# Optimization experiments

Hardware: AMD Instinct MI355X
Metric: run time of the kernel (lower is better)

## Reference

```python
import jax, jax.numpy as jnp
import numpy as np

N_NODES = 100000
N_FEAT = 256
HIDDEN = 16
N_CLASSES = 16
N_EDGES = 3200000


def setup_inputs() -> dict:
    key = jax.random.key(0)
    k = jax.random.split(key, 7)
    x = jax.random.normal(k[0], (N_NODES, N_FEAT), dtype=jnp.float32)
    edge_index = jax.random.randint(k[1], (2, N_EDGES), 0, N_NODES, dtype=jnp.int32)
    # GCNConv: linear (no bias) + bias added after aggregation
    s1 = 1.0 / np.sqrt(N_FEAT)
    W1 = jax.random.uniform(k[2], (N_FEAT, HIDDEN), jnp.float32, -s1, s1)
    b1 = jnp.zeros((HIDDEN,), jnp.float32)
    # SAGEConv: lin_l (on aggregated neighbors, with bias) + lin_r (root)
    s2 = 1.0 / np.sqrt(HIDDEN)
    Wl = jax.random.uniform(k[3], (HIDDEN, N_CLASSES), jnp.float32, -s2, s2)
    Wr = jax.random.uniform(k[4], (HIDDEN, N_CLASSES), jnp.float32, -s2, s2)
    b2 = jax.random.uniform(k[5], (N_CLASSES,), jnp.float32, -s2, s2)
    return {"x": x, "edge_index": edge_index, "W1": W1, "b1": b1,
            "Wl": Wl, "Wr": Wr, "b2": b2}


def reference(x, edge_index, W1, b1, Wl, Wr, b2):
    N = x.shape[0]
    src, dst = edge_index[0], edge_index[1]

    # ---- GCNConv(num_features -> hidden): transform, add self-loops,
    # symmetric normalization, sum-aggregate, add bias ----
    h = x @ W1  # [N, H]
    loop = jnp.arange(N, dtype=src.dtype)
    src2 = jnp.concatenate([src, loop])
    dst2 = jnp.concatenate([dst, loop])
    ones = jnp.ones(src2.shape[0], dtype=h.dtype)
    deg = jax.ops.segment_sum(ones, dst2, num_segments=N)  # in-degree incl. self-loop
    dinv = jnp.where(deg > 0, jax.lax.rsqrt(deg), 0.0)
    norm = dinv[src2] * dinv[dst2]  # [E+N]
    msgs = h[src2] * norm[:, None]
    h1 = jax.ops.segment_sum(msgs, dst2, num_segments=N) + b1  # [N, H]

    # ---- SAGEConv(hidden -> num_classes, aggr='mean') ----
    cnt = jax.ops.segment_sum(jnp.ones(src.shape[0], dtype=h1.dtype), dst, num_segments=N)
    agg = jax.ops.segment_sum(h1[src], dst, num_segments=N)
    agg = agg / jnp.maximum(cnt, 1.0)[:, None]  # mean over neighbors
    out = agg @ Wl + h1 @ Wr + b2  # [N, C]

    return jax.nn.log_softmax(out, axis=1)
```

## Files before the change

### kernel.cpp

```cpp
#include <hip/hip_runtime.h>
#include <cstddef>

#define NF 256
#define NH 16
#define NC 16

#define BN    128
#define BSH   7
#define BMSK  127
#define CAP   4608
#define AVLEN 16
#define ACH   (256*AVLEN)
#define NBMAX 800

typedef __attribute__((ext_vector_type(8))) short bf16x8;
typedef __attribute__((ext_vector_type(4))) float f32x4;

__device__ inline short f2bf(float f) {
    union { float f; unsigned int u; } v; v.f = f;
    const unsigned int r = v.u + 0x7FFFu + ((v.u >> 16) & 1u);
    return (short)(r >> 16);
}
__device__ inline float bf2f(unsigned short u) {
    union { unsigned int i; float f; } v; v.i = ((unsigned int)u) << 16;
    return v.f;
}

__global__ __launch_bounds__(256) void fusedAG_kernel(
    const int* __restrict__ src, const int* __restrict__ dst,
    unsigned int* __restrict__ bfill, unsigned int* __restrict__ bpairs,
    const float* __restrict__ x, const float* __restrict__ W1,
    float* __restrict__ hs_u, int E, int NBK, int NCH, int GEMMB, int N)
{
    __shared__ unsigned int hist[NBMAX];
    __shared__ unsigned int sbase[NBMAX];
    __shared__ unsigned int reorder[ACH];
    __shared__ unsigned short wbid[ACH];
    __shared__ unsigned int wsum[4];

    const int tid = threadIdx.x;

    const int nInter = 2 * (NCH < GEMMB ? NCH : GEMMB);
    int msId = -1, gbId = -1;
    const int bi = (int)blockIdx.x;
    if (bi < nInter) {
        if (bi & 1) gbId = bi >> 1; else msId = bi >> 1;
    } else {
        const int r = bi - nInter;
        if (NCH > GEMMB) msId = (nInter >> 1) + r; else gbId = (nInter >> 1) + r;
    }

    if (msId >= 0) {
        for (int i = tid; i < NBMAX; i += 256) hist[i] = 0u;
        __syncthreads();

        const int base = msId * ACH;
        unsigned int pv[AVLEN];
        unsigned int ps[AVLEN];
        #pragma unroll
        for (int l = 0; l < AVLEN; ++l) {
            const int e = base + l * 256 + tid;
            if (e < E) {
                const unsigned int s = (unsigned int)src[e];
                const unsigned int d = (unsigned int)dst[e];
                const unsigned int b = d >> BSH;
                pv[l] = (s << BSH) | (d & BMSK);
                const unsigned int slot = atomicAdd(&hist[b], 1u);
                ps[l] = (slot << 10) | b;
            } else {
                ps[l] = 0xFFFFFFFFu;
            }
        }
        __syncthreads();

        {
            const int lane = tid & 63;
            const int wid  = tid >> 6;
            const int b0 = tid * 4;
            unsigned int h0 = (b0 + 0 < NBMAX) ? hist[b0 + 0] : 0u;
            unsigned int h1 = (b0 + 1 < NBMAX) ? hist[b0 + 1] : 0u;
            unsigned int h2 = (b0 + 2 < NBMAX) ? hist[b0 + 2] : 0u;
            unsigned int h3 = (b0 + 3 < NBMAX) ? hist[b0 + 3] : 0u;
            const unsigned int l0 = h0, l1 = l0 + h1, l2 = l1 + h2;
            const unsigned int s = l2 + h3;
            unsigned int ws = s;
            #pragma unroll
            for (int d = 1; d < 64; d <<= 1) {
                const unsigned int v = __shfl_up(ws, d, 64);
                if (lane >= d) ws += v;
            }
            if (lane == 63) wsum[wid] = ws;
            __syncthreads();
            unsigned int woff = 0;
            #pragma unroll
            for (int w = 0; w < 4; ++w) woff += (w < wid) ? wsum[w] : 0u;
            const unsigned int ebase = woff + (ws - s);
            if (b0 + 0 < NBMAX) sbase[b0 + 0] = ebase;
            if (b0 + 1 < NBMAX) sbase[b0 + 1] = ebase + l0;
            if (b0 + 2 < NBMAX) sbase[b0 + 2] = ebase + l1;
            if (b0 + 3 < NBMAX) sbase[b0 + 3] = ebase + l2;
        }
        const int cc = (base + ACH <= E) ? ACH : (E - base);
        __syncthreads();

        #pragma unroll
        for (int l = 0; l < AVLEN; ++l) {
            if (ps[l] != 0xFFFFFFFFu) {
                const unsigned int b = ps[l] & 1023u;
                const unsigned int i = sbase[b] + (ps[l] >> 10);
                reorder[i] = pv[l];
                wbid[i] = (unsigned short)b;
            }
        }
        __syncthreads();

        for (int i = tid; i < NBK; i += 256) {
            const unsigned int h = hist[i];
            const unsigned int g = h ? atomicAdd(&bfill[i], h) : 0u;
            hist[i] = g - sbase[i];
        }
        __syncthreads();

        for (int i = tid; i < cc; i += 256) {
            const unsigned int b = wbid[i];
            const unsigned int g = hist[b] + (unsigned int)i;
            if (g < CAP) bpairs[(size_t)b * CAP + g] = reorder[i];
        }
    } else {
        const int lane = tid & 63;
        const int wave = tid >> 6;
        const int quad = lane >> 4;
        const int mn   = lane & 15;

        bf16x8 bfrag[8];
        #pragma unroll
        for (int kc = 0; kc < 8; ++kc) {
            #pragma unroll
            for (int j = 0; j < 8; ++j) {
                const int k = kc * 32 + quad * 8 + j;
                bfrag[kc][j] = f2bf(W1[k * NH + mn]);
            }
        }

        #pragma unroll
        for (int t = 0; t < 2; ++t) {
            const int tile = gbId * 8 + wave * 2 + t;
            const int n0 = tile * 16;
            if (n0 >= N) break;

            f32x4 acc = {0.f, 0.f, 0.f, 0.f};
            const float* xrow = x + (size_t)(n0 + mn) * NF + quad * 8;
            #pragma unroll
            for (int kc = 0; kc < 8; ++kc) {
                const float4 lo = *(const float4*)(xrow + kc * 32);
                const float4 hi = *(const float4*)(xrow + kc * 32 + 4);
                bf16x8 af;
                af[0] = f2bf(lo.x); af[1] = f2bf(lo.y); af[2] = f2bf(lo.z); af[3] = f2bf(lo.w);
                af[4] = f2bf(hi.x); af[5] = f2bf(hi.y); af[6] = f2bf(hi.z); af[7] = f2bf(hi.w);
                acc = __builtin_amdgcn_mfma_f32_16x16x32_bf16(af, bfrag[kc], acc, 0, 0, 0);
            }

            #pragma unroll
            for (int r = 0; r < 4; ++r) {
                const int row = quad * 4 + r;
                hs_u[(size_t)(n0 + row) * NH + mn] = acc[r];
            }
        }
    }
}

__global__ __launch_bounds__(256) void bucketB_kernel(
    const unsigned int* __restrict__ bfill, unsigned int* __restrict__ bpairs,
    const float* __restrict__ hs_u,
    int* __restrict__ rowptr, int* __restrict__ cnt, float* __restrict__ dinv,
    unsigned short* __restrict__ hs_bf, int N)
{
    __shared__ unsigned int pairs[CAP];
    __shared__ unsigned int ssorted[CAP];
    __shared__ unsigned int hist[BN];
    __shared__ unsigned int scan[BN];
    __shared__ unsigned int cursor[BN];
    __shared__ float sdinv[BN];

    const int tid = threadIdx.x;
    const int b = blockIdx.x;
    const size_t bbase = (size_t)b * CAP;
    const int nodeBase = b * BN;
    unsigned int m = bfill[b]; if (m > CAP) m = CAP;

    if (tid < BN) hist[tid] = 0u;
    __syncthreads();

    for (unsigned int i = tid; i < m; i += 256) {
        const unsigned int p = bpairs[bbase + i];
        pairs[i] = p;
        atomicAdd(&hist[p & BMSK], 1u);
    }
    __syncthreads();

    if (tid < BN) scan[tid] = hist[tid];
    __syncthreads();
    for (int off = 1; off < BN; off <<= 1) {
        unsigned int v = 0;
        if (tid < BN && tid >= off) v = scan[tid - off];
        __syncthreads();
        if (tid < BN) scan[tid] += v;
        __syncthreads();
    }
    if (tid < BN) cursor[tid] = scan[tid] - hist[tid];
    __syncthreads();

    for (unsigned int i = tid; i < m; i += 256) {
        const unsigned int p = pairs[i];
        const unsigned int pos = atomicAdd(&cursor[p & BMSK], 1u);
        ssorted[pos] = p >> BSH;
    }
    __syncthreads();

    for (unsigned int i = tid; i < m; i += 256)
        bpairs[bbase + i] = ssorted[i];

    if (tid < BN) {
        const int n = nodeBase + tid;
        const unsigned int h = hist[tid];
        const float dv = rsqrtf((float)h + 1.0f);
        sdinv[tid] = dv;
        if (n < N) {
            cnt[n] = (int)h;
            dinv[n] = dv;
            rowptr[n] = (int)(b * CAP + (scan[tid] - h));
        }
    }
    __syncthreads();

    for (int t = tid; t < BN * NH; t += 256) {
        const int n = nodeBase + (t >> 4);
        if (n < N) {
            const size_t idx = (size_t)n * NH + (t & 15);
            hs_bf[idx] = (unsigned short)f2bf(hs_u[idx] * sdinv[t >> 4]);
        }
    }
}

__global__ __launch_bounds__(256) void gcn_gather_kernel(
    const unsigned short* __restrict__ hs_bf, const unsigned int* __restrict__ csrc,
    const int* __restrict__ rowptr, const int* __restrict__ cnt,
    const float* __restrict__ dinv, const float* __restrict__ b1,
    unsigned short* __restrict__ h1_bf, int N)
{
    const int tid = threadIdx.x;
    const int n = blockIdx.x * 16 + (tid >> 4);
    if (n >= N) return;
    const int j  = tid & 15;
    const int q  = j & 3;
    const int es = j >> 2;
    const int start = rowptr[n];
    const int end = start + cnt[n];

    f32x4 acc = {0.f, 0.f, 0.f, 0.f};
    for (int k = start; k < end; k += 16) {
        const int idx = k + j;
        const int myi = (int)csrc[idx < end ? idx : (end - 1)];
        #pragma unroll
        for (int s = 0; s < 4; ++s) {
            const int e = s * 4 + es;
            const int sidx = __shfl(myi, e, 16);
            const ushort4 r = *reinterpret_cast<const ushort4*>(
                hs_bf + (size_t)sidx * NH + q * 4);
            if (k + e < end) {
                acc[0] += bf2f(r.x); acc[1] += bf2f(r.y);
                acc[2] += bf2f(r.z); acc[3] += bf2f(r.w);
            }
        }
    }
    #pragma unroll
    for (int c = 0; c < 4; ++c) {
        acc[c] += __shfl_xor(acc[c], 4, 16);
        acc[c] += __shfl_xor(acc[c], 8, 16);
    }

    if (j < 4) {
        const ushort4 sr = *reinterpret_cast<const ushort4*>(
            hs_bf + (size_t)n * NH + j * 4);
        const float dv = dinv[n];
        ushort4 o;
        o.x = (unsigned short)f2bf(b1[j * 4 + 0] + dv * (acc[0] + bf2f(sr.x)));
        o.y = (unsigned short)f2bf(b1[j * 4 + 1] + dv * (acc[1] + bf2f(sr.y)));
        o.z = (unsigned short)f2bf(b1[j * 4 + 2] + dv * (acc[2] + bf2f(sr.z)));
        o.w = (unsigned short)f2bf(b1[j * 4 + 3] + dv * (acc[3] + bf2f(sr.w)));
        *reinterpret_cast<ushort4*>(h1_bf + (size_t)n * NH + j * 4) = o;
    }
}

__global__ __launch_bounds__(256) void sage_out_kernel(
    const unsigned short* __restrict__ h1_bf, const unsigned int* __restrict__ csrc,
    const int* __restrict__ rowptr, const int* __restrict__ cnt,
    const float* __restrict__ Wl, const float* __restrict__ Wr,
    const float* __restrict__ b2, float* __restrict__ out, int N)
{
    __shared__ float wls[NH * NC];
    __shared__ float wrs[NH * NC];
    __shared__ float b2s[NC];
    __shared__ float sagg[16][NH];
    const int tid = threadIdx.x;
    if (tid < NH * NC) { wls[tid] = Wl[tid]; wrs[tid] = Wr[tid]; }
    if (tid < NC) b2s[tid] = b2[tid];
    __syncthreads();

    const int g = tid >> 4;
    const int n = blockIdx.x * 16 + g;
    if (n >= N) return;
    const int j  = tid & 15;
    const int q  = j & 3;
    const int es = j >> 2;
    const int start = rowptr[n];
    const int deg = cnt[n];
    const int end = start + deg;

    f32x4 acc = {0.f, 0.f, 0.f, 0.f};
    for (int k = start; k < end; k += 16) {
        const int idx = k + j;
        const int myi = (int)csrc[idx < end ? idx : (end - 1)];
        #pragma unroll
        for (int s = 0; s < 4; ++s) {
            const int e = s * 4 + es;
            const int sidx = __shfl(myi, e, 16);
            const ushort4 r = *reinterpret_cast<const ushort4*>(
                h1_bf + (size_t)sidx * NH + q * 4);
            if (k + e < end) {
                acc[0] += bf2f(r.x); acc[1] += bf2f(r.y);
                acc[2] += bf2f(r.z); acc[3] += bf2f(r.w);
            }
        }
    }
    #pragma unroll
    for (int c = 0; c < 4; ++c) {
        acc[c] += __shfl_xor(acc[c], 4, 16);
        acc[c] += __shfl_xor(acc[c], 8, 16);
    }

    const float inv = 1.0f / fmaxf((float)deg, 1.0f);
    if (j < 4) {
        sagg[g][j * 4 + 0] = acc[0] * inv;
        sagg[g][j * 4 + 1] = acc[1] * inv;
        sagg[g][j * 4 + 2] = acc[2] * inv;
        sagg[g][j * 4 + 3] = acc[3] * inv;
    }

    const float h1j = bf2f(h1_bf[(size_t)n * NH + j]);

    float o = b2s[j];
    #pragma unroll
    for (int kk = 0; kk < NH; ++kk) {
        const float a  = sagg[g][kk];
        const float hh = __shfl(h1j, kk, 16);
        o += a * wls[kk * NC + j] + hh * wrs[kk * NC + j];
    }

    float m = o;
    #pragma unroll
    for (int off = 1; off < 16; off <<= 1) m = fmaxf(m, __shfl_xor(m, off, 16));
    const float ex = expf(o - m);
    float ssum = ex;
    #pragma unroll
    for (int off = 1; off < 16; off <<= 1) ssum += __shfl_xor(ssum, off, 16);

    out[(size_t)n * NC + j] = (o - m) - logf(ssum);
}

extern "C" void kernel_launch(void* const* d_in, const int* in_sizes, int n_in,
                              void* d_out, int out_size, void* d_ws, size_t ws_size,
                              hipStream_t stream)
{
    const float* x  = (const float*)d_in[0];
    const int*   ei = (const int*)d_in[1];
    const float* W1 = (const float*)d_in[2];
    const float* b1 = (const float*)d_in[3];
    const float* Wl = (const float*)d_in[4];
    const float* Wr = (const float*)d_in[5];
    const float* b2 = (const float*)d_in[6];
    float* out = (float*)d_out;

    const int N = in_sizes[0] / NF;
    const int E = in_sizes[1] / 2;
    const int* src = ei;
    const int* dst = ei + E;

    const int NBK = (N + BN - 1) / BN;
    const int NCH = (E + ACH - 1) / ACH;
    const int tiles = (N + 15) / 16;
    const int GEMMB = (tiles + 7) / 8;

    unsigned short* hs_bf = (unsigned short*)d_ws;
    unsigned short* h1_bf = hs_bf + (size_t)N * NH;
    float* hs_u   = (float*)(h1_bf + (size_t)N * NH);
    float* dinv   = hs_u + (size_t)N * NH;
    int*   cnt    = (int*)(dinv + N);
    int*   rowptr = cnt + N;
    unsigned int* bfill  = (unsigned int*)(rowptr + N);
    unsigned int* bpairs = bfill + 1024;

    hipMemsetAsync(bfill, 0, (size_t)NBK * sizeof(unsigned int), stream);

    fusedAG_kernel<<<NCH + GEMMB, 256, 0, stream>>>(
        src, dst, bfill, bpairs, x, W1, hs_u, E, NBK, NCH, GEMMB, N);
    bucketB_kernel<<<NBK, 256, 0, stream>>>(
        bfill, bpairs, hs_u, rowptr, cnt, dinv, hs_bf, N);

    const int nodeBlk = (N + 15) / 16;
    gcn_gather_kernel<<<nodeBlk, 256, 0, stream>>>(hs_bf, bpairs, rowptr, cnt, dinv, b1, h1_bf, N);
    sage_out_kernel<<<nodeBlk, 256, 0, stream>>>(h1_bf, bpairs, rowptr, cnt, Wl, Wr, b2, out, N);
}
```

Measured before the change: 278.0 us.

## Fuse bucket sort, GCN gather and SAGE output into one cooperative kernel

Merges the bucket-sort, GCN aggregation and SAGE/log-softmax kernels into a single cooperative kernel with one block per 128-node bucket. Each block keeps its sorted source indices in LDS, and grid.sync separates the phases. This removes two kernel launches, the global write-back of sorted pairs and the rowptr/cnt/dinv arrays, and the prefix scan now uses wave shuffles. The cost is that a cooperative launch needs all ~782 blocks to be co-resident, with large LDS per block. Each 16-lane group also now processes 8 nodes serially, which lowers parallelism and load balance.

After: 577.0 us. 108% more time.

```diff
diff --git a/kernel.cpp b/kernel.cpp
--- a/kernel.cpp
+++ b/kernel.cpp
@@ -1,5 +1,8 @@
 #include <hip/hip_runtime.h>
+#include <hip/hip_cooperative_groups.h>
 #include <cstddef>
+
+namespace cg = cooperative_groups;
 
 #define NF 256
 #define NH 16
@@ -169,69 +172,63 @@
     }
 }
 
-__global__ __launch_bounds__(256) void bucketB_kernel(
-    const unsigned int* __restrict__ bfill, unsigned int* __restrict__ bpairs,
-    const float* __restrict__ hs_u,
-    int* __restrict__ rowptr, int* __restrict__ cnt, float* __restrict__ dinv,
-    unsigned short* __restrict__ hs_bf, int N)
+__global__ __launch_bounds__(256) void fusedBCD_kernel(
+    const unsigned int* __restrict__ bfill, const unsigned int* __restrict__ bpairs,
+    const float* __restrict__ hs_u, const float* __restrict__ b1,
+    const float* __restrict__ Wl, const float* __restrict__ Wr,
+    const float* __restrict__ b2,
+    unsigned short* __restrict__ hs_bf, unsigned short* __restrict__ h1_bf,
+    float* __restrict__ out, int N)
 {
-    __shared__ unsigned int pairs[CAP];
     __shared__ unsigned int ssorted[CAP];
     __shared__ unsigned int hist[BN];
     __shared__ unsigned int scan[BN];
     __shared__ unsigned int cursor[BN];
     __shared__ float sdinv[BN];
-
+    __shared__ float wls[NH * NC];
+    __shared__ float wrs[NH * NC];
+    __shared__ float b2s[NC];
+    __shared__ float sagg[16][NH];
+
+    cg::grid_group grid = cg::this_grid();
     const int tid = threadIdx.x;
     const int b = blockIdx.x;
     const size_t bbase = (size_t)b * CAP;
     const int nodeBase = b * BN;
     unsigned int m = bfill[b]; if (m > CAP) m = CAP;
 
+    if (tid < NH * NC) { wls[tid] = Wl[tid]; wrs[tid] = Wr[tid]; }
+    if (tid < NC) b2s[tid] = b2[tid];
     if (tid < BN) hist[tid] = 0u;
     __syncthreads();
 
+    for (unsigned int i = tid; i < m; i += 256)
+        atomicAdd(&hist[bpairs[bbase + i] & BMSK], 1u);
+    __syncthreads();
+
+    if (tid < 64) {
+        const unsigned int h0 = hist[2 * tid], h1 = hist[2 * tid + 1];
+        const unsigned int s = h0 + h1;
+        unsigned int ws = s;
+        #pragma unroll
+        for (int d = 1; d < 64; d <<= 1) {
+            const unsigned int v = __shfl_up(ws, d, 64);
+            if (tid >= d) ws += v;
+        }
+        scan[2 * tid]     = ws - h1;
+        scan[2 * tid + 1] = ws;
+        cursor[2 * tid]     = ws - s;
+        cursor[2 * tid + 1] = ws - h1;
+        sdinv[2 * tid]     = rsqrtf((float)h0 + 1.0f);
+        sdinv[2 * tid + 1] = rsqrtf((float)h1 + 1.0f);
+    }
+    __syncthreads();
+
     for (unsigned int i = tid; i < m; i += 256) {
         const unsigned int p = bpairs[bbase + i];
-        pairs[i] = p;
-        atomicAdd(&hist[p & BMSK], 1u);
-    }
-    __syncthreads();
-
-    if (tid < BN) scan[tid] = hist[tid];
-    __syncthreads();
-    for (int off = 1; off < BN; off <<= 1) {
-        unsigned int v = 0;
-        if (tid < BN && tid >= off) v = scan[tid - off];
-        __syncthreads();
-        if (tid < BN) scan[tid] += v;
-        __syncthreads();
-    }
-    if (tid < BN) cursor[tid] = scan[tid] - hist[tid];
-    __syncthreads();
-
-    for (unsigned int i = tid; i < m; i += 256) {
-        const unsigned int p = pairs[i];
         const unsigned int pos = atomicAdd(&cursor[p & BMSK], 1u);
         ssorted[pos] = p >> BSH;
     }
-    __syncthreads();
-
-    for (unsigned int i = tid; i < m; i += 256)
-        bpairs[bbase + i] = ssorted[i];
-
-    if (tid < BN) {
-        const int n = nodeBase + tid;
-        const unsigned int h = hist[tid];
-        const float dv = rsqrtf((float)h + 1.0f);
-        sdinv[tid] = dv;
-        if (n < N) {
-            cnt[n] = (int)h;
-            dinv[n] = dv;
-            rowptr[n] = (int)(b * CAP + (scan[tid] - h));
-        }
-    }
-    __syncthreads();
 
     for (int t = tid; t < BN * NH; t += 256) {
         const int n = nodeBase + (t >> 4);
@@ -240,132 +237,110 @@
             hs_bf[idx] = (unsigned short)f2bf(hs_u[idx] * sdinv[t >> 4]);
         }
     }
-}
-
-__global__ __launch_bounds__(256) void gcn_gather_kernel(
-    const unsigned short* __restrict__ hs_bf, const unsigned int* __restrict__ csrc,
-    const int* __restrict__ rowptr, const int* __restrict__ cnt,
-    const float* __restrict__ dinv, const float* __restrict__ b1,
-    unsigned short* __restrict__ h1_bf, int N)
-{
-    const int tid = threadIdx.x;
-    const int n = blockIdx.x * 16 + (tid >> 4);
-    if (n >= N) return;
+
+    __threadfence();
+    grid.sync();
+
+    const int g  = tid >> 4;
     const int j  = tid & 15;
     const int q  = j & 3;
     const int es = j >> 2;
-    const int start = rowptr[n];
-    const int end = start + cnt[n];
-
-    f32x4 acc = {0.f, 0.f, 0.f, 0.f};
-    for (int k = start; k < end; k += 16) {
-        const int idx = k + j;
-        const int myi = (int)csrc[idx < end ? idx : (end - 1)];
-        #pragma unroll
-        for (int s = 0; s < 4; ++s) {
-            const int e = s * 4 + es;
-            const int sidx = __shfl(myi, e, 16);
-            const ushort4 r = *reinterpret_cast<const ushort4*>(
-                hs_bf + (size_t)sidx * NH + q * 4);
-            if (k + e < end) {
-                acc[0] += bf2f(r.x); acc[1] += bf2f(r.y);
-                acc[2] += bf2f(r.z); acc[3] += bf2f(r.w);
-            }
-        }
-    }
-    #pragma unroll
-    for (int c = 0; c < 4; ++c) {
-        acc[c] += __shfl_xor(acc[c], 4, 16);
-        acc[c] += __shfl_xor(acc[c], 8, 16);
-    }
-
-    if (j < 4) {
-        const ushort4 sr = *reinterpret_cast<const ushort4*>(
-            hs_bf + (size_t)n * NH + j * 4);
-        const float dv = dinv[n];
-        ushort4 o;
-        o.x = (unsigned short)f2bf(b1[j * 4 + 0] + dv * (acc[0] + bf2f(sr.x)));
-        o.y = (unsigned short)f2bf(b1[j * 4 + 1] + dv * (acc[1] + bf2f(sr.y)));
-        o.z = (unsigned short)f2bf(b1[j * 4 + 2] + dv * (acc[2] + bf2f(sr.z)));
-        o.w = (unsigned short)f2bf(b1[j * 4 + 3] + dv * (acc[3] + bf2f(sr.w)));
-        *reinterpret_cast<ushort4*>(h1_bf + (size_t)n * NH + j * 4) = o;
-    }
-}
-
-__global__ __launch_bounds__(256) void sage_out_kernel(
-    const unsigned short* __restrict__ h1_bf, const unsigned int* __restrict__ csrc,
-    const int* __restrict__ rowptr, const int* __restrict__ cnt,
-    const float* __restrict__ Wl, const float* __restrict__ Wr,
-    const float* __restrict__ b2, float* __restrict__ out, int N)
-{
-    __shared__ float wls[NH * NC];
-    __shared__ float wrs[NH * NC];
-    __shared__ float b2s[NC];
-    __shared__ float sagg[16][NH];
-    const int tid = threadIdx.x;
-    if (tid < NH * NC) { wls[tid] = Wl[tid]; wrs[tid] = Wr[tid]; }
-    if (tid < NC) b2s[tid] = b2[tid];
-    __syncthreads();
-
-    const int g = tid >> 4;
-    const int n = blockIdx.x * 16 + g;
-    if (n >= N) return;
-    const int j  = tid & 15;
-    const int q  = j & 3;
-    const int es = j >> 2;
-    const int start = rowptr[n];
-    const int deg = cnt[n];
-    const int end = start + deg;
-
-    f32x4 acc = {0.f, 0.f, 0.f, 0.f};
-    for (int k = start; k < end; k += 16) {
-        const int idx = k + j;
-        const int myi = (int)csrc[idx < end ? idx : (end - 1)];
-        #pragma unroll
-        for (int s = 0; s < 4; ++s) {
-            const int e = s * 4 + es;
-            const int sidx = __shfl(myi, e, 16);
-            const ushort4 r = *reinterpret_cast<const ushort4*>(
-                h1_bf + (size_t)sidx * NH + q * 4);
-            if (k + e < end) {
-                acc[0] += bf2f(r.x); acc[1] += bf2f(r.y);
-                acc[2] += bf2f(r.z); acc[3] += bf2f(r.w);
-            }
-        }
-    }
-    #pragma unroll
-    for (int c = 0; c < 4; ++c) {
-        acc[c] += __shfl_xor(acc[c], 4, 16);
-        acc[c] += __shfl_xor(acc[c], 8, 16);
-    }
-
-    const float inv = 1.0f / fmaxf((float)deg, 1.0f);
-    if (j < 4) {
-        sagg[g][j * 4 + 0] = acc[0] * inv;
-        sagg[g][j * 4 + 1] = acc[1] * inv;
-        sagg[g][j * 4 + 2] = acc[2] * inv;
-        sagg[g][j * 4 + 3] = acc[3] * inv;
-    }
-
-    const float h1j = bf2f(h1_bf[(size_t)n * NH + j]);
-
-    float o = b2s[j];
-    #pragma unroll
-    for (int kk = 0; kk < NH; ++kk) {
-        const float a  = sagg[g][kk];
-        const float hh = __shfl(h1j, kk, 16);
-        o += a * wls[kk * NC + j] + hh * wrs[kk * NC + j];
-    }
-
-    float m = o;
-    #pragma unroll
-    for (int off = 1; off < 16; off <<= 1) m = fmaxf(m, __shfl_xor(m, off, 16));
-    const float ex = expf(o - m);
-    float ssum = ex;
-    #pragma unroll
-    for (int off = 1; off < 16; off <<= 1) ssum += __shfl_xor(ssum, off, 16);
-
-    out[(size_t)n * NC + j] = (o - m) - logf(ssum);
+
+    for (int t = 0; t < 8; ++t) {
+        const int ln = g * 8 + t;
+        const int n = nodeBase + ln;
+        if (n >= N) continue;
+        const int deg  = (int)hist[ln];
+        const int base = (int)(scan[ln] - hist[ln]);
+
+        f32x4 acc = {0.f, 0.f, 0.f, 0.f};
+        for (int k = 0; k < deg; k += 16) {
+            #pragma unroll
+            for (int s = 0; s < 4; ++s) {
+                const int e = k + s * 4 + es;
+                const int sidx = (int)ssorted[base + (e < deg ? e : deg - 1)];
+                const ushort4 r = *reinterpret_cast<const ushort4*>(
+                    hs_bf + (size_t)sidx * NH + q * 4);
+                if (e < deg) {
+                    acc[0] += bf2f(r.x); acc[1] += bf2f(r.y);
+                    acc[2] += bf2f(r.z); acc[3] += bf2f(r.w);
+                }
+            }
+        }
+        #pragma unroll
+        for (int c = 0; c < 4; ++c) {
+            acc[c] += __shfl_xor(acc[c], 4, 16);
+            acc[c] += __shfl_xor(acc[c], 8, 16);
+        }
+        if (j < 4) {
+            const ushort4 sr = *reinterpret_cast<const ushort4*>(
+                hs_bf + (size_t)n * NH + j * 4);
+            const float dv = sdinv[ln];
+            ushort4 o;
+            o.x = (unsigned short)f2bf(b1[j * 4 + 0] + dv * (acc[0] + bf2f(sr.x)));
+            o.y = (unsigned short)f2bf(b1[j * 4 + 1] + dv * (acc[1] + bf2f(sr.y)));
+            o.z = (unsigned short)f2bf(b1[j * 4 + 2] + dv * (acc[2] + bf2f(sr.z)));
+            o.w = (unsigned short)f2bf(b1[j * 4 + 3] + dv * (acc[3] + bf2f(sr.w)));
+            *reinterpret_cast<ushort4*>(h1_bf + (size_t)n * NH + j * 4) = o;
+        }
+    }
+
+    __threadfence();
+    grid.sync();
+
+    for (int t = 0; t < 8; ++t) {
+        const int ln = g * 8 + t;
+        const int n = nodeBase + ln;
+        if (n >= N) continue;
+        const int deg  = (int)hist[ln];
+        const int base = (int)(scan[ln] - hist[ln]);
+
+        f32x4 acc = {0.f, 0.f, 0.f, 0.f};
+        for (int k = 0; k < deg; k += 16) {
+            #pragma unroll
+            for (int s = 0; s < 4; ++s) {
+                const int e = k + s * 4 + es;
+                const int sidx = (int)ssorted[base + (e < deg ? e : deg - 1)];
+                const ushort4 r = *reinterpret_cast<const ushort4*>(
+                    h1_bf + (size_t)sidx * NH + q * 4);
+                if (e < deg) {
+                    acc[0] += bf2f(r.x); acc[1] += bf2f(r.y);
+                    acc[2] += bf2f(r.z); acc[3] += bf2f(r.w);
+                }
+            }
+        }
+        #pragma unroll
+        for (int c = 0; c < 4; ++c) {
+            acc[c] += __shfl_xor(acc[c], 4, 16);
+            acc[c] += __shfl_xor(acc[c], 8, 16);
+        }
+
+        const float inv = 1.0f / fmaxf((float)deg, 1.0f);
+        if (j < 4) {
+            sagg[g][j * 4 + 0] = acc[0] * inv;
+            sagg[g][j * 4 + 1] = acc[1] * inv;
+            sagg[g][j * 4 + 2] = acc[2] * inv;
+            sagg[g][j * 4 + 3] = acc[3] * inv;
+        }
+        __builtin_amdgcn_wave_barrier();
+
+        const float h1j = bf2f(h1_bf[(size_t)n * NH + j]);
+        float o = b2s[j];
+        #pragma unroll
+        for (int kk = 0; kk < NH; ++kk) {
+            o += sagg[g][kk] * wls[kk * NC + j] + __shfl(h1j, kk, 16) * wrs[kk * NC + j];
+        }
+
+        float mx = o;
+        #pragma unroll
+        for (int off = 1; off < 16; off <<= 1) mx = fmaxf(mx, __shfl_xor(mx, off, 16));
+        const float ex = expf(o - mx);
+        float ssum = ex;
+        #pragma unroll
+        for (int off = 1; off < 16; off <<= 1) ssum += __shfl_xor(ssum, off, 16);
+
+        out[(size_t)n * NC + j] = (o - mx) - logf(ssum);
+    }
 }
 
 extern "C" void kernel_launch(void* const* d_in, const int* in_sizes, int n_in,
@@ -394,20 +369,21 @@
     unsigned short* hs_bf = (unsigned short*)d_ws;
     unsigned short* h1_bf = hs_bf + (size_t)N * NH;
     float* hs_u   = (float*)(h1_bf + (size_t)N * NH);
-    float* dinv   = hs_u + (size_t)N * NH;
-    int*   cnt    = (int*)(dinv + N);
-    int*   rowptr = cnt + N;
-    unsigned int* bfill  = (unsigned int*)(rowptr + N);
+    unsigned int* bfill  = (unsigned int*)(hs_u + (size_t)N * NH);
     unsigned int* bpairs = bfill + 1024;
 
-    hipMemsetAsync(bfill, 0, (size_t)NBK * sizeof(unsigned int), stream);
+    hipMemsetAsync(bfill, 0, 1024 * sizeof(unsigned int), stream);
 
     fusedAG_kernel<<<NCH + GEMMB, 256, 0, stream>>>(
         src, dst, bfill, bpairs, x, W1, hs_u, E, NBK, NCH, GEMMB, N);
-    bucketB_kernel<<<NBK, 256, 0, stream>>>(
-        bfill, bpairs, hs_u, rowptr, cnt, dinv, hs_bf, N);
-
-    const int nodeBlk = (N + 15) / 16;
-    gcn_gather_kernel<<<nodeBlk, 256, 0, stream>>>(hs_bf, bpairs, rowptr, cnt, dinv, b1, h1_bf, N);
-    sage_out_kernel<<<nodeBlk, 256, 0, stream>>>(h1_bf, bpairs, rowptr, cnt, Wl, Wr, b2, out, N);
-}
+
+    {
+        void* kargs[] = {
+            (void*)&bfill, (void*)&bpairs, (void*)&hs_u, (void*)&b1,
+            (void*)&Wl, (void*)&Wr, (void*)&b2,
+            (void*)&hs_bf, (void*)&h1_bf, (void*)&out, (void*)&N
+        };
+        hipLaunchCooperativeKernel((void*)fusedBCD_kernel, dim3(NBK), dim3(256),
+                                   kargs, 0, stream);
+    }
+}
```
